# Performance work log

Hardware: AMD Instinct MI355X
Metric: run time of the kernel (lower is better)

The kernel has to match this reference:

```python
import jax, jax.numpy as jnp
import numpy as np

B, T, D = 64, 512, 41  # batch, target timesteps, channels (input_dim)


def setup_inputs() -> dict:
    key = jax.random.key(0)
    k1, k2, k3 = jax.random.split(key, 3)
    target_x = jax.random.uniform(k1, (B, T), dtype=jnp.float32)
    vals = jax.random.normal(k2, (B, T, D), dtype=jnp.float32)
    mask = jax.random.randint(k3, (B, T, D), 0, 2, dtype=jnp.int32)
    return {"target_x": target_x, "vals": vals, "mask": mask}


def reference(target_x, vals, mask):
    # Faithful vectorized version of TRIPLETFORMER.compute_unsupervised_loss's
    # ragged target assembly (the torch code loops over the batch with boolean
    # indexing + F.pad; here we left-pack with a stable argsort on the mask).
    b, t, d = vals.shape
    L = t * d  # full_len = tau.size(1) * self.dim

    tau = jnp.broadcast_to(target_x[:, :, None], (b, t, d)).reshape(b, L)
    U = vals.reshape(b, L)
    mk = mask.reshape(b, L)
    # C = cumsum(ones, -1) - 1 over channel axis == arange(d) broadcast
    C = jnp.broadcast_to(jnp.arange(d, dtype=jnp.int32), (b, t, d)).reshape(b, L)

    # Stable sort: observed entries (mk==1) packed to the front, order preserved.
    order = jnp.argsort(1 - mk, axis=-1, stable=True)  # [B, L]
    take = lambda x: jnp.take_along_axis(x, order, axis=-1)

    mk_p = take(mk)                                   # sorted mask: 1s then 0s
    valid = mk_p.astype(tau.dtype)
    tau_p = take(tau) * valid                         # pad with 0, as F.pad(value=0)
    U_p = take(U) * valid
    C_p = take(C) * mk_p                              # padded C entries -> 0 (matches torch pad)

    C_onehot = jax.nn.one_hot(C_p, d, dtype=tau.dtype)            # [B, L, D]
    target_context = jnp.concatenate([tau_p[:, :, None], C_onehot], -1)  # [B, L, 1+D]
    # target_mask = stack([C_, mk], -1); target_vals = U packed.
    # (The data-dependent obs_len truncation in torch is a pure slice of zero
    #  rows; omitted here to keep static shapes — values are identical.)
    out = jnp.concatenate(
        [target_context,                # [:, :, :1+D]  tau + one-hot channel
         U_p[:, :, None],               # packed target values
         valid[:, :, None]],            # packed observation mask
        axis=-1)                        # [B, L, D+3]
    return out
```

## Files before the change

### kernel.cpp

```cpp
#include <hip/hip_runtime.h>

#define BB 64
#define TT 512
#define DD 41
#define LL (TT * DD)
#define COLS (DD + 3)
#define F4R (COLS / 4)
#define TILE 256
#define TPB (LL / TILE)
#define NTILES (BB * TPB)

typedef float f4v __attribute__((ext_vector_type(4)));


__global__ __launch_bounds__(TILE)
void k1_count(const int* __restrict__ mask, int* __restrict__ partials) {
    const int blk = blockIdx.x;
    const int tid = threadIdx.x;
    const int m = mask[(size_t)blk * TILE + tid];
    const unsigned long long bal = __ballot(m != 0);
    __shared__ int ws[4];
    if ((tid & 63) == 0) ws[tid >> 6] = __popcll(bal);
    __syncthreads();
    if (tid == 0) partials[blk] = ws[0] + ws[1] + ws[2] + ws[3];
}

__global__ __launch_bounds__(128)
void k2_scan(const int* __restrict__ partials, int* __restrict__ tileOff,
             int* __restrict__ nObs) {
    const int b   = blockIdx.x;
    const int tid = threadIdx.x;
    const int v = (tid < TPB) ? partials[b * TPB + tid] : 0;
    __shared__ int s[128];
    s[tid] = v;
    __syncthreads();
    for (int off = 1; off < 128; off <<= 1) {
        const int t = (tid >= off) ? s[tid - off] : 0;
        __syncthreads();
        s[tid] += t;
        __syncthreads();
    }
    if (tid < TPB) tileOff[b * TPB + tid] = s[tid] - v;
    if (tid == TPB - 1) nObs[b] = s[tid];
}

__global__ __launch_bounds__(TILE)
void k3_emit(const float* __restrict__ target_x, const float* __restrict__ vals,
             const int* __restrict__ mask, const int* __restrict__ tileOff,
             const int* __restrict__ nObs, float* __restrict__ out) {
    const int blk = blockIdx.x;
    const int tid = threadIdx.x;
    const int b     = blk / TPB;
    const int lrow0 = (blk - b * TPB) * TILE;
    const size_t src = (size_t)blk * TILE + tid;

    const int   m    = mask[src] != 0;
    const float Uraw = vals[src];
    const int lrow = lrow0 + tid;
    const int t  = lrow / DD;
    const int ch = lrow - t * DD;
    const float tau = target_x[b * TT + t];

    const unsigned long long bal = __ballot(m);
    const int lane = tid & 63;
    const int w    = tid >> 6;
    const int rankInWave = __popcll(bal & ((1ull << lane) - 1ull));
    __shared__ int wsum[4];
    if (lane == 0) wsum[w] = __popcll(bal);
    __syncthreads();
    const int s0 = wsum[0], s1 = wsum[1], s2 = wsum[2], s3 = wsum[3];
    const int cntObs = s0 + s1 + s2 + s3;
    const int wbase  = (w > 0 ? s0 : 0) + (w > 1 ? s1 : 0) + (w > 2 ? s2 : 0);
    const int eObs = wbase + rankInWave;
    const int d = m ? eObs : cntObs + (tid - eObs);

    __shared__ f4v info[TILE];
    f4v inf;
    inf.x = m ? tau : 0.0f;
    inf.y = m ? Uraw : 0.0f;
    inf.z = __int_as_float(m ? ch : 0);
    inf.w = m ? 1.0f : 0.0f;
    info[d] = inf;
    __syncthreads();

    const int tOff    = tileOff[blk];
    const int padRow0 = nObs[b] + (lrow0 - tOff);
    const size_t rowBase = (size_t)b * LL;

    f4v* outp = reinterpret_cast<f4v*>(out);
#pragma unroll
    for (int k = 0; k < F4R; ++k) {
        const int q  = k * TILE + tid;
        const int rr = q / F4R;
        const int c4 = q - rr * F4R;
        const f4v v = info[rr];
        const int chh = __float_as_int(v.z);
        const int gr = (rr < cntObs) ? (tOff + rr) : (padRow0 + (rr - cntObs));
        const int c0 = c4 * 4;
        f4v rv;
#pragma unroll
        for (int j = 0; j < 4; ++j) {
            const int c = c0 + j;
            float x;
            if (c == 0)            x = v.x;
            else if (c <= DD)      x = (c - 1 == chh) ? 1.0f : 0.0f;
            else if (c == DD + 1)  x = v.y;
            else                   x = v.w;
            rv[j] = x;
        }
        outp[(rowBase + (size_t)gr) * F4R + c4] = rv;
    }
}

extern "C" void kernel_launch(void* const* d_in, const int* in_sizes, int n_in,
                              void* d_out, int out_size, void* d_ws, size_t ws_size,
                              hipStream_t stream) {
    const float* target_x = (const float*)d_in[0];
    const float* vals     = (const float*)d_in[1];
    const int*   mask     = (const int*)d_in[2];
    float* out = (float*)d_out;

    int* partials = (int*)d_ws;
    int* tileOff  = partials + NTILES;
    int* nObs     = tileOff + NTILES;

    k1_count<<<NTILES, TILE, 0, stream>>>(mask, partials);
    k2_scan<<<BB, 128, 0, stream>>>(partials, tileOff, nObs);
    k3_emit<<<NTILES, TILE, 0, stream>>>(target_x, vals, mask, tileOff, nObs, out);
}
```

Baseline: 247.4 us.

## Fuse count and scan kernels, pass mask bitmap to emit kernel

Merges the per-tile mask count and the per-batch scan into one kernel with one block per batch row, which also writes a compact ballot bitmap of the mask. The emit kernel then reads that bitmap instead of the int32 mask and computes ranks without a ballot or block barrier. This drops one launch and a second full read of the mask. In exchange the count phase runs on only 64 blocks, each looping over 82 tiles, so the mask read has much less parallelism.

Result: slower. 254.3 us (+2.8%).

```diff
diff --git a/kernel.cpp b/kernel.cpp
--- a/kernel.cpp
+++ b/kernel.cpp
@@ -11,68 +11,84 @@
 #define NTILES (BB * TPB)
 
 typedef float f4v __attribute__((ext_vector_type(4)));
+typedef unsigned long long u64;
 
 
-__global__ __launch_bounds__(TILE)
-void k1_count(const int* __restrict__ mask, int* __restrict__ partials) {
-    const int blk = blockIdx.x;
-    const int tid = threadIdx.x;
-    const int m = mask[(size_t)blk * TILE + tid];
-    const unsigned long long bal = __ballot(m != 0);
-    __shared__ int ws[4];
-    if ((tid & 63) == 0) ws[tid >> 6] = __popcll(bal);
+__global__ __launch_bounds__(256)
+void kA_count_scan(const int* __restrict__ mask, u64* __restrict__ bitmap,
+                   int* __restrict__ tileOff, int* __restrict__ nObs) {
+    const int b    = blockIdx.x;
+    const int tid  = threadIdx.x;
+    const int w    = tid >> 6;
+    const int lane = tid & 63;
+    const int* mrow = mask + (size_t)b * LL;
+
+    __shared__ int cnts[TPB];
+    __shared__ int s[256];
+
+    for (int it = 0; it < 21; ++it) {
+        const int tile = it * 4 + w;
+        if (tile < TPB) {
+            u64 bal[4];
+            int cnt = 0;
+#pragma unroll
+            for (int j = 0; j < 4; ++j) {
+                const int m = mrow[tile * TILE + j * 64 + lane];
+                bal[j] = __ballot(m != 0);
+                cnt += __popcll(bal[j]);
+            }
+            if (lane == 0) {
+#pragma unroll
+                for (int j = 0; j < 4; ++j)
+                    bitmap[(size_t)(b * TPB + tile) * 4 + j] = bal[j];
+                cnts[tile] = cnt;
+            }
+        }
+    }
     __syncthreads();
-    if (tid == 0) partials[blk] = ws[0] + ws[1] + ws[2] + ws[3];
-}
 
-__global__ __launch_bounds__(128)
-void k2_scan(const int* __restrict__ partials, int* __restrict__ tileOff,
-             int* __restrict__ nObs) {
-    const int b   = blockIdx.x;
-    const int tid = threadIdx.x;
-    const int v = (tid < TPB) ? partials[b * TPB + tid] : 0;
-    __shared__ int s[128];
+    const int v = (tid < TPB) ? cnts[tid] : 0;
     s[tid] = v;
     __syncthreads();
-    for (int off = 1; off < 128; off <<= 1) {
+    for (int off = 1; off < 256; off <<= 1) {
         const int t = (tid >= off) ? s[tid - off] : 0;
         __syncthreads();
         s[tid] += t;
         __syncthreads();
     }
     if (tid < TPB) tileOff[b * TPB + tid] = s[tid] - v;
-    if (tid == TPB - 1) nObs[b] = s[tid];
+    if (tid == 0)  nObs[b] = s[TPB - 1];
 }
 
 __global__ __launch_bounds__(TILE)
-void k3_emit(const float* __restrict__ target_x, const float* __restrict__ vals,
-             const int* __restrict__ mask, const int* __restrict__ tileOff,
+void kB_emit(const float* __restrict__ target_x, const float* __restrict__ vals,
+             const u64* __restrict__ bitmap, const int* __restrict__ tileOff,
              const int* __restrict__ nObs, float* __restrict__ out) {
     const int blk = blockIdx.x;
     const int tid = threadIdx.x;
     const int b     = blk / TPB;
     const int lrow0 = (blk - b * TPB) * TILE;
-    const size_t src = (size_t)blk * TILE + tid;
+    const int w     = tid >> 6;
+    const int lane  = tid & 63;
 
-    const int   m    = mask[src] != 0;
-    const float Uraw = vals[src];
+    const u64 b0 = bitmap[(size_t)blk * 4 + 0];
+    const u64 b1 = bitmap[(size_t)blk * 4 + 1];
+    const u64 b2 = bitmap[(size_t)blk * 4 + 2];
+    const u64 b3 = bitmap[(size_t)blk * 4 + 3];
+    const u64 mybal = (w == 0) ? b0 : (w == 1) ? b1 : (w == 2) ? b2 : b3;
+
+    const int m = (int)((mybal >> lane) & 1ull);
+    const int p0 = __popcll(b0), p1 = __popcll(b1), p2 = __popcll(b2), p3 = __popcll(b3);
+    const int cntObs = p0 + p1 + p2 + p3;
+    const int wbase  = (w > 0 ? p0 : 0) + (w > 1 ? p1 : 0) + (w > 2 ? p2 : 0);
+    const int eObs   = wbase + __popcll(mybal & ((1ull << lane) - 1ull));
+    const int d = m ? eObs : cntObs + (tid - eObs);
+
+    const float Uraw = vals[(size_t)blk * TILE + tid];
     const int lrow = lrow0 + tid;
     const int t  = lrow / DD;
     const int ch = lrow - t * DD;
     const float tau = target_x[b * TT + t];
-
-    const unsigned long long bal = __ballot(m);
-    const int lane = tid & 63;
-    const int w    = tid >> 6;
-    const int rankInWave = __popcll(bal & ((1ull << lane) - 1ull));
-    __shared__ int wsum[4];
-    if (lane == 0) wsum[w] = __popcll(bal);
-    __syncthreads();
-    const int s0 = wsum[0], s1 = wsum[1], s2 = wsum[2], s3 = wsum[3];
-    const int cntObs = s0 + s1 + s2 + s3;
-    const int wbase  = (w > 0 ? s0 : 0) + (w > 1 ? s1 : 0) + (w > 2 ? s2 : 0);
-    const int eObs = wbase + rankInWave;
-    const int d = m ? eObs : cntObs + (tid - eObs);
 
     __shared__ f4v info[TILE];
     f4v inf;
@@ -120,11 +136,10 @@
     const int*   mask     = (const int*)d_in[2];
     float* out = (float*)d_out;
 
-    int* partials = (int*)d_ws;
-    int* tileOff  = partials + NTILES;
-    int* nObs     = tileOff + NTILES;
+    u64* bitmap  = (u64*)d_ws;
+    int* tileOff = (int*)(bitmap + (size_t)NTILES * 4);
+    int* nObs    = tileOff + NTILES;
 
-    k1_count<<<NTILES, TILE, 0, stream>>>(mask, partials);
-    k2_scan<<<BB, 128, 0, stream>>>(partials, tileOff, nObs);
-    k3_emit<<<NTILES, TILE, 0, stream>>>(target_x, vals, mask, tileOff, nObs, out);
+    kA_count_scan<<<BB, 256, 0, stream>>>(mask, bitmap, tileOff, nObs);
+    kB_emit<<<NTILES, TILE, 0, stream>>>(target_x, vals, bitmap, tileOff, nObs, out);
 }
```
